# Kernel optimization log

Hardware: AMD Instinct MI355X
Metric: run time of the kernel (lower is better)

Reference implementation:

```python
import jax, jax.numpy as jnp
import numpy as np

N = 20000          # nodes
DEG = 8            # deterministic in-degree per node
E = N * DEG        # edges
IN_DIM = 16
HID = 128
EDGE_DIM = 8
OUT_DIM = 4
LN_EPS = 1e-5
# degree histogram has all mass at DEG -> avg log-degree = log(DEG + 1)
AVG_DEG_LOG = float(np.log(DEG + 1.0))


def _init(key, fan_in, fan_out):
    s = float(np.sqrt(2.0 / (fan_in + fan_out)))  # glorot-ish
    return jax.random.normal(key, (fan_in, fan_out), jnp.float32) * s


def setup_inputs() -> dict:
    key = jax.random.key(0)
    ks = jax.random.split(key, 24)
    x = jax.random.normal(ks[0], (N, IN_DIM), jnp.float32)
    src = jax.random.randint(ks[1], (E,), 0, N, jnp.int32)
    dst = (jnp.arange(E, dtype=jnp.int32) % N)  # every node has exactly DEG in-edges
    edge_index = jnp.stack([src, dst], axis=0)
    edge_attr = jax.random.normal(ks[2], (E, EDGE_DIM), jnp.float32)
    d = {"x": x, "edge_attr": edge_attr, "edge_index": edge_index}
    i = 3
    for l, fi in enumerate([IN_DIM, HID]):  # 2 PNAConv layers (num_layers=3)
        d[f"ew{l}"] = _init(ks[i], EDGE_DIM, fi); i += 1   # edge_encoder
        d[f"eb{l}"] = jnp.zeros((fi,), jnp.float32)
        d[f"pw{l}"] = _init(ks[i], 3 * fi, fi); i += 1     # pre_nn: cat(x_i,x_j,e)
        d[f"pb{l}"] = jnp.zeros((fi,), jnp.float32)
        d[f"qw{l}"] = _init(ks[i], 13 * fi, HID); i += 1   # post_nn: (4 aggr * 3 scalers + 1)*F_in
        d[f"qb{l}"] = jnp.zeros((HID,), jnp.float32)
        d[f"lw{l}"] = _init(ks[i], HID, HID); i += 1       # PNAConv.lin
        d[f"lb{l}"] = jnp.zeros((HID,), jnp.float32)
        d[f"g{l}"] = jnp.ones((HID,), jnp.float32)         # LayerNorm gamma
        d[f"b{l}"] = jnp.zeros((HID,), jnp.float32)        # LayerNorm beta
    d["hw"] = _init(ks[i], HID, OUT_DIM)
    d["hb"] = jnp.zeros((OUT_DIM,), jnp.float32)
    return d


def _pna_conv(x, src, dst, edge_attr, ew, eb, pw, pb, qw, qb, lw, lb):
    # messages: cat(x_i, x_j, edge_encoder(edge_attr)) -> pre MLP
    e = edge_attr @ ew + eb                                   # [E, F_in]
    h = jnp.concatenate([x[dst], x[src], e], axis=-1)         # [E, 3*F_in]
    h = h @ pw + pb                                           # [E, F_in]
    # multi-aggregator reduce by destination node
    deg = jax.ops.segment_sum(jnp.ones((E,), h.dtype), dst, num_segments=N)
    degc = jnp.maximum(deg, 1.0)[:, None]
    mean = jax.ops.segment_sum(h, dst, num_segments=N) / degc
    mean2 = jax.ops.segment_sum(h * h, dst, num_segments=N) / degc
    mx = jax.ops.segment_max(h, dst, num_segments=N)
    mn = jax.ops.segment_min(h, dst, num_segments=N)
    std = jnp.sqrt(jax.nn.relu(mean2 - mean * mean) + 1e-5)
    agg = jnp.concatenate([mean, mx, mn, std], axis=-1)       # [N, 4*F_in]
    # degree scalers: identity, amplification, attenuation (scaler-major layout)
    logd = jnp.log(deg + 1.0)[:, None]
    scaled = jnp.concatenate(
        [agg, agg * (logd / AVG_DEG_LOG), agg * (AVG_DEG_LOG / logd)], axis=-1
    )                                                         # [N, 12*F_in]
    out = jnp.concatenate([x, scaled], axis=-1) @ qw + qb     # post_nn, [N, F_out]
    return out @ lw + lb                                      # PNAConv.lin


def _ln(x, g, b):
    m = jnp.mean(x, axis=-1, keepdims=True)
    v = jnp.mean((x - m) ** 2, axis=-1, keepdims=True)
    return (x - m) / jnp.sqrt(v + LN_EPS) * g + b


def reference(x, edge_attr, ew0, eb0, pw0, pb0, qw0, qb0, lw0, lb0, g0, b0,
              ew1, eb1, pw1, pb1, qw1, qb1, lw1, lb1, g1, b1, hw, hb, edge_index):
    src, dst = edge_index[0], edge_index[1]
    h = _pna_conv(x, src, dst, edge_attr, ew0, eb0, pw0, pb0, qw0, qb0, lw0, lb0)
    h = jax.nn.relu(_ln(h, g0, b0))  # dropout is identity at inference
    h = _pna_conv(h, src, dst, edge_attr, ew1, eb1, pw1, pb1, qw1, qb1, lw1, lb1)
    h = jax.nn.relu(_ln(h, g1, b1))
    return h @ hw + hb               # head, [N, OUT_DIM]
```

## Files before the change

kernel.cpp:

```cpp
#include <hip/hip_runtime.h>
#include <math.h>

#define N_NODES 20000
#define N_EDGES 160000

typedef unsigned short ushort_t;
typedef __attribute__((ext_vector_type(8))) short short8v;
typedef __attribute__((ext_vector_type(4))) float f32x4;
typedef __attribute__((ext_vector_type(8))) float f32x8;

#define WS_We0  0
#define WS_b0m  128
#define WS_W0   256
#define WS_b0   10496
#define WS_We1  10624
#define WS_b1m  11648
#define WS_b1   11776
#define WS_WP1  11904
#define WS_WPTU 52864
#define WS_t0   69248
#define WS_u0   389248
#define WS_h0b  709248
#define WS_t1   1989248
#define WS_u1   4549248
#define WS_A0   7109248
#define WS_A1   7109248

__device__ inline ushort_t f2bf(float f) {
    union { float f; unsigned u; } v; v.f = f;
    unsigned r = v.u + 0x7FFFu + ((v.u >> 16) & 1u);
    return (ushort_t)(r >> 16);
}

__device__ __attribute__((noinline)) void prep_item(
    int tid, const float* __restrict__ x,
    const float* __restrict__ ew0, const float* __restrict__ eb0,
    const float* __restrict__ pw0, const float* __restrict__ pb0,
    const float* __restrict__ qw0, const float* __restrict__ qb0,
    const float* __restrict__ lw0, const float* __restrict__ lb0,
    const float* __restrict__ ew1, const float* __restrict__ eb1,
    const float* __restrict__ pw1, const float* __restrict__ pb1,
    const float* __restrict__ qw1, const float* __restrict__ qb1,
    const float* __restrict__ lw1, const float* __restrict__ lb1,
    float* __restrict__ ws)
{
    if (tid < 81920) {
        int r = tid >> 7, o = tid & 127;
        float acc = 0.f;
        for (int h = 0; h < 128; ++h) {
            float qr;
            if (r < 128) qr = qw1[r*128 + h];
            else {
                int s = r - 128;
                qr = qw1[(128+s)*128+h] + qw1[(640+s)*128+h] + qw1[(1152+s)*128+h];
            }
            acc += qr * lw1[h*128 + o];
        }
        int ct = o >> 4, ks = r >> 5;
        int l = (o & 15) | (((r >> 3) & 3) << 4);
        ((ushort_t*)(ws + WS_WP1))[(size_t)(((ct*20 + ks)*64) + l)*8 + (r & 7)] = f2bf(acc);
    } else if (tid < 82048) {
        int o = tid - 81920;
        float acc = lb1[o];
        for (int h = 0; h < 128; ++h) acc += qb1[h] * lw1[h*128 + o];
        ws[WS_b1 + o] = acc;
    } else if (tid < 92288) {
        int idx = tid - 82048; int r = idx >> 7, o = idx & 127;
        float acc = 0.f;
        for (int h = 0; h < 128; ++h) {
            float qr;
            if (r < 16) qr = qw0[r*128 + h];
            else {
                int s = r - 16;
                qr = qw0[(16+s)*128+h] + qw0[(80+s)*128+h] + qw0[(144+s)*128+h];
            }
            acc += qr * lw0[h*128 + o];
        }
        ws[WS_W0 + idx] = acc;
    } else if (tid < 92416) {
        int o = tid - 92288;
        float acc = lb0[o];
        for (int h = 0; h < 128; ++h) acc += qb0[h] * lw0[h*128 + o];
        ws[WS_b0 + o] = acc;
    } else if (tid < 93440) {
        int idx = tid - 92416; int c = idx >> 7, f = idx & 127;
        float acc = 0.f;
        for (int k = 0; k < 128; ++k) acc += ew1[c*128 + k] * pw1[(256+k)*128 + f];
        ws[WS_We1 + idx] = acc;
    } else if (tid < 93568) {
        int f = tid - 93440;
        float acc = pb1[f];
        for (int k = 0; k < 128; ++k) acc += eb1[k] * pw1[(256+k)*128 + f];
        ws[WS_b1m + f] = acc;
    } else if (tid < 93696) {
        int idx = tid - 93568; int c = idx >> 4, f = idx & 15;
        float acc = 0.f;
        for (int k = 0; k < 16; ++k) acc += ew0[c*16 + k] * pw0[(32+k)*16 + f];
        ws[WS_We0 + idx] = acc;
    } else if (tid < 93712) {
        int f = tid - 93696;
        float acc = pb0[f];
        for (int k = 0; k < 16; ++k) acc += eb0[k] * pw0[(32+k)*16 + f];
        ws[WS_b0m + f] = acc;
    } else if (tid < 126480) {
        int idx = tid - 93712;
        int r = idx >> 7, o = idx & 127;
        int part = r >> 7, rk = r & 127;
        int ct = part*8 + (o >> 4);
        int l = (o & 15) | (((rk >> 3) & 3) << 4);
        ((ushort_t*)(ws + WS_WPTU))[(size_t)(((ct*4 + (rk >> 5))*64) + l)*8 + (rk & 7)]
            = f2bf(pw1[r*128 + o]);
    } else if (tid < 446480) {
        int idx = tid - 126480; int i = idx >> 4, f = idx & 15;
        float acc = 0.f;
        for (int k = 0; k < 16; ++k) acc += x[i*16 + k] * pw0[k*16 + f];
        ws[WS_t0 + idx] = acc;
    } else if (tid < 766480) {
        int idx = tid - 446480; int i = idx >> 4, f = idx & 15;
        float acc = 0.f;
        for (int k = 0; k < 16; ++k) acc += x[i*16 + k] * pw0[(16+k)*16 + f];
        ws[WS_u0 + idx] = acc;
    }
}

__device__ __attribute__((noinline)) void agg0_tile(
    int tile, int t, const float* __restrict__ x, const float* __restrict__ ea,
    const int* __restrict__ src, float* __restrict__ ws)
{
    static __shared__ float ea_s0[16*8*8];
    static __shared__ int   src_s0[16*8];
    static __shared__ float We0_s0[128];
    static __shared__ float b0m_s0[16];
    const int i0 = tile * 16;
    __syncthreads();

    for (int idx = t; idx < 1024; idx += 256) {
        int k = idx >> 7; int rem = idx & 127; int n = rem >> 3, c = rem & 7;
        ea_s0[(n*8 + k)*8 + c] = ea[(i0 + n + k*N_NODES)*8 + c];
    }
    if (t < 128) {
        int k = t >> 4, n = t & 15;
        src_s0[n*8 + k] = src[i0 + n + k*N_NODES];
        We0_s0[t] = ws[WS_We0 + t];
    }
    if (t < 16) b0m_s0[t] = ws[WS_b0m + t];
    __syncthreads();

    const int n = t >> 4, f = t & 15;
    const int i = i0 + n;
    float base = ws[WS_t0 + i*16 + f] + b0m_s0[f];
    float s = 0.f, q = 0.f, mx = -1e30f, mn = 1e30f;
    for (int k = 0; k < 8; ++k) {
        int sj = src_s0[n*8 + k];
        float m = base + ws[WS_u0 + sj*16 + f];
        #pragma unroll
        for (int c = 0; c < 8; ++c) m += ea_s0[(n*8+k)*8 + c] * We0_s0[c*16 + f];
        s += m; q += m*m; mx = fmaxf(mx, m); mn = fminf(mn, m);
    }
    float mean = s * 0.125f, mean2 = q * 0.125f;
    float sd = sqrtf(fmaxf(mean2 - mean*mean, 0.f) + 1e-5f);
    float* A0 = ws + WS_A0 + (size_t)i * 80;
    A0[f]      = x[i*16 + f];
    A0[16 + f] = mean;
    A0[32 + f] = mx;
    A0[48 + f] = mn;
    A0[64 + f] = sd;
}

__device__ __attribute__((noinline)) void gemm0_tile(
    int tile, int t, const float* __restrict__ g0, const float* __restrict__ bln0,
    float* __restrict__ ws)
{
    static __shared__ float As[32][81];
    const int r0 = tile * 32;
    __syncthreads();
    const float* A = ws + WS_A0 + (size_t)r0 * 80;
    for (int idx = t; idx < 32*80; idx += 256) {
        int r = idx / 80, k = idx - r*80;
        As[r][k] = A[idx];
    }
    __syncthreads();
    const int tc = t & 31, tr = t >> 5;
    const int c0 = tc * 4;
    float acc[4][4] = {};
    const float* W = ws + WS_W0;
    #pragma unroll 4
    for (int k = 0; k < 80; ++k) {
        float4 b = *(const float4*)(W + k*128 + c0);
        #pragma unroll
        for (int rr = 0; rr < 4; ++rr) {
            float a = As[tr*4 + rr][k];
            acc[rr][0] += a*b.x; acc[rr][1] += a*b.y;
            acc[rr][2] += a*b.z; acc[rr][3] += a*b.w;
        }
    }
    float4 bias = *(const float4*)(ws + WS_b0 + c0);
    float4 g  = *(const float4*)(g0 + c0);
    float4 bb = *(const float4*)(bln0 + c0);
    ushort_t* h0b = (ushort_t*)(ws + WS_h0b);
    #pragma unroll
    for (int rr = 0; rr < 4; ++rr) {
        float v0 = acc[rr][0] + bias.x, v1 = acc[rr][1] + bias.y;
        float v2 = acc[rr][2] + bias.z, v3 = acc[rr][3] + bias.w;
        float sum = v0+v1+v2+v3;
        float sq  = v0*v0+v1*v1+v2*v2+v3*v3;
        #pragma unroll
        for (int off = 1; off < 32; off <<= 1) {
            sum += __shfl_xor(sum, off, 64);
            sq  += __shfl_xor(sq,  off, 64);
        }
        float mean = sum * (1.f/128.f);
        float var  = sq  * (1.f/128.f) - mean*mean;
        float rstd = rsqrtf(var + 1e-5f);
        ushort4 ob;
        ob.x = f2bf(fmaxf((v0-mean)*rstd*g.x + bb.x, 0.f));
        ob.y = f2bf(fmaxf((v1-mean)*rstd*g.y + bb.y, 0.f));
        ob.z = f2bf(fmaxf((v2-mean)*rstd*g.z + bb.z, 0.f));
        ob.w = f2bf(fmaxf((v3-mean)*rstd*g.w + bb.w, 0.f));
        *(ushort4*)(h0b + (size_t)(r0 + tr*4 + rr)*128 + c0) = ob;
    }
}

__device__ __attribute__((noinline)) void tu1_half(
    int tile, int part, int lane, float* __restrict__ ws)
{
    const int rowbase = tile * 16;
    const ushort_t* h0b = (const ushort_t*)(ws + WS_h0b);
    const ushort_t* WP  = (const ushort_t*)(ws + WS_WPTU);
    const int lr = lane & 15, lk = lane >> 4;
    const size_t arow = rowbase + lr;
    f32x4 acc[8];
    #pragma unroll
    for (int c = 0; c < 8; ++c) acc[c] = (f32x4){0.f,0.f,0.f,0.f};

    #pragma unroll
    for (int ks = 0; ks < 4; ++ks) {
        short8v a = *(const short8v*)(h0b + arow*128 + ks*32 + lk*8);
        #pragma unroll
        for (int c = 0; c < 8; ++c) {
            short8v b = *(const short8v*)(WP + ((size_t)((part*8 + c)*4 + ks)*64 + lane)*8);
            acc[c] = __builtin_amdgcn_mfma_f32_16x16x32_bf16(a, b, acc[c], 0, 0, 0);
        }
    }
    float* dst = part ? (ws + WS_u1) : (ws + WS_t1);
    #pragma unroll
    for (int c = 0; c < 8; ++c) {
        int cb = c*16 + lr;
        #pragma unroll
        for (int r = 0; r < 4; ++r) {
            int row = rowbase + lk*4 + r;
            dst[(size_t)row*128 + cb] = acc[c][r];
        }
    }
}

__device__ __attribute__((noinline)) void agg1_tile(
    int tile, int t, const float* __restrict__ ea, const int* __restrict__ src,
    float* __restrict__ ws)
{
    static __shared__ float ea_s1[16*8*8];
    static __shared__ int   src_s1[128];
    static __shared__ float We1_s1[1024];
    static __shared__ float b1m_s1[128];
    const int i0 = tile * 16;
    __syncthreads();

    for (int idx = t; idx < 1024; idx += 256) {
        int k = idx >> 7; int rem = idx & 127; int n = rem >> 3, c = rem & 7;
        ea_s1[(n*8 + k)*8 + c] = ea[(i0 + n + k*N_NODES)*8 + c];
    }
    if (t < 128) {
        int k = t >> 4, n = t & 15;
        src_s1[n*8 + k] = src[i0 + n + k*N_NODES];
    }
    for (int idx = t; idx < 1024; idx += 256) We1_s1[idx] = ws[WS_We1 + idx];
    if (t < 128) b1m_s1[t] = ws[WS_b1m + t];
    __syncthreads();

    const int n = t >> 4, f0 = (t & 15) * 8;
    const int i = i0 + n;
    float base[8], sm[8], sq[8], mx[8], mn[8];
    #pragma unroll
    for (int e = 0; e < 8; ++e) {
        base[e] = ws[WS_t1 + (size_t)i*128 + f0 + e] + b1m_s1[f0 + e];
        sm[e] = 0.f; sq[e] = 0.f; mx[e] = -1e30f; mn[e] = 1e30f;
    }
    for (int k = 0; k < 8; ++k) {
        int sj = src_s1[n*8 + k];
        const float* urow = ws + WS_u1 + (size_t)sj*128 + f0;
        float m[8];
        #pragma unroll
        for (int e = 0; e < 8; ++e) m[e] = base[e] + urow[e];
        #pragma unroll
        for (int c = 0; c < 8; ++c) {
            float a = ea_s1[(n*8 + k)*8 + c];
            #pragma unroll
            for (int e = 0; e < 8; ++e) m[e] += a * We1_s1[c*128 + f0 + e];
        }
        #pragma unroll
        for (int e = 0; e < 8; ++e) {
            sm[e] += m[e]; sq[e] += m[e]*m[e];
            mx[e] = fmaxf(mx[e], m[e]); mn[e] = fminf(mn[e], m[e]);
        }
    }
    ushort_t* A1 = (ushort_t*)(ws + WS_A1);
    short8v vm, vx, vn, vs;
    #pragma unroll
    for (int e = 0; e < 8; ++e) {
        float mean = sm[e]*0.125f, m2 = sq[e]*0.125f;
        float sd = sqrtf(fmaxf(m2 - mean*mean, 0.f) + 1e-5f);
        vm[e] = (short)f2bf(mean);
        vx[e] = (short)f2bf(mx[e]);
        vn[e] = (short)f2bf(mn[e]);
        vs[e] = (short)f2bf(sd);
    }
    size_t b = (size_t)i*512 + f0;
    *(short8v*)(A1 + b)       = vm;
    *(short8v*)(A1 + b + 128) = vx;
    *(short8v*)(A1 + b + 256) = vn;
    *(short8v*)(A1 + b + 384) = vs;
}

__device__ __attribute__((noinline)) void gemm1_tile(
    int tile, int tl, int hf,
    const float* __restrict__ g1, const float* __restrict__ bln1,
    const float* __restrict__ hw, const float* __restrict__ hb,
    float* __restrict__ ws, float* __restrict__ out)
{
    static __shared__ float redS[2][2][16], redQ[2][2][16];
    static __shared__ f32x4 redP[2][16];
    const int w = tl >> 6, lane = tl & 63;
    const int lr = lane & 15, lk = lane >> 4;
    const int rowbase = tile * 16;
    const int row = rowbase + lr;
    const ushort_t* h0b = (const ushort_t*)(ws + WS_h0b);
    const ushort_t* A1  = (const ushort_t*)(ws + WS_A1);
    const ushort_t* WP  = (const ushort_t*)(ws + WS_WP1);

    f32x4 acc[4];
    #pragma unroll
    for (int c = 0; c < 4; ++c) acc[c] = (f32x4){0.f,0.f,0.f,0.f};

    #pragma unroll
    for (int kw = 0; kw < 4; ++kw) {
        short8v a = *(const short8v*)(h0b + (size_t)row*128 + kw*32 + lk*8);
        #pragma unroll
        for (int c = 0; c < 4; ++c) {
            int ct = w*4 + c;
            short8v b = *(const short8v*)(WP + (size_t)((ct*20 + kw)*64 + lane)*8);
            acc[c] = __builtin_amdgcn_mfma_f32_16x16x32_bf16(a, b, acc[c], 0, 0, 0);
        }
    }
    #pragma unroll 4
    for (int ks = 0; ks < 16; ++ks) {
        short8v a = *(const short8v*)(A1 + (size_t)row*512 + ks*32 + lk*8);
        #pragma unroll
        for (int c = 0; c < 4; ++c) {
            int ct = w*4 + c;
            short8v b = *(const short8v*)(WP + (size_t)((ct*20 + 4 + ks)*64 + lane)*8);
            acc[c] = __builtin_amdgcn_mfma_f32_16x16x32_bf16(a, b, acc[c], 0, 0, 0);
        }
    }

    float bc[4], gc[4], bbc[4]; f32x4 hwc[4];
    #pragma unroll
    for (int c = 0; c < 4; ++c) {
        int col = (w*4 + c)*16 + lr;
        bc[c]  = ws[WS_b1 + col];
        gc[c]  = g1[col];
        bbc[c] = bln1[col];
        hwc[c] = *(const f32x4*)(hw + col*4);
    }

    #pragma unroll
    for (int r = 0; r < 4; ++r) {
        float s = 0.f, q = 0.f;
        #pragma unroll
        for (int c = 0; c < 4; ++c) {
            float v = acc[c][r] + bc[c];
            s += v; q += v*v;
        }
        #pragma unroll
        for (int off = 1; off < 16; off <<= 1) {
            s += __shfl_xor(s, off, 64);
            q += __shfl_xor(q, off, 64);
        }
        if (lr == 0) { redS[hf][w][lk*4 + r] = s; redQ[hf][w][lk*4 + r] = q; }
    }
    __syncthreads();

    f32x4 poarr[4];
    #pragma unroll
    for (int r = 0; r < 4; ++r) {
        int orow = lk*4 + r;
        float s_tot = redS[hf][0][orow] + redS[hf][1][orow];
        float q_tot = redQ[hf][0][orow] + redQ[hf][1][orow];
        float mean = s_tot * (1.f/128.f);
        float var  = q_tot * (1.f/128.f) - mean*mean;
        float rstd = rsqrtf(var + 1e-5f);
        f32x4 po = (f32x4){0.f,0.f,0.f,0.f};
        #pragma unroll
        for (int c = 0; c < 4; ++c) {
            float v = acc[c][r] + bc[c];
            float o = fmaxf((v-mean)*rstd*gc[c] + bbc[c], 0.f);
            po += o * hwc[c];
        }
        #pragma unroll
        for (int off = 1; off < 16; off <<= 1) {
            po.x += __shfl_xor(po.x, off, 64);
            po.y += __shfl_xor(po.y, off, 64);
            po.z += __shfl_xor(po.z, off, 64);
            po.w += __shfl_xor(po.w, off, 64);
        }
        poarr[r] = po;
        if (w == 1 && lr == 0) redP[hf][orow] = po;
    }
    __syncthreads();

    if (w == 0 && lr == 0) {
        f32x4 hb4 = *(const f32x4*)hb;
        #pragma unroll
        for (int r = 0; r < 4; ++r) {
            int orow = lk*4 + r;
            f32x4 res = poarr[r] + redP[hf][orow] + hb4;
            *(f32x4*)(out + (size_t)(rowbase + orow)*4) = res;
        }
    }
}

struct KArgs {
    const float *x, *ea; const int* src;
    const float *ew0,*eb0,*pw0,*pb0,*qw0,*qb0,*lw0,*lb0,*g0,*bl0;
    const float *ew1,*eb1,*pw1,*pb1,*qw1,*qb1,*lw1,*lb1,*g1,*bl1;
    const float *hw,*hb;
    float* ws; float* out;
};

__global__ __launch_bounds__(256) void k_prep(KArgs a) {
    int tid = blockIdx.x*256 + threadIdx.x;
    prep_item(tid, a.x, a.ew0, a.eb0, a.pw0, a.pb0, a.qw0, a.qb0, a.lw0, a.lb0,
              a.ew1, a.eb1, a.pw1, a.pb1, a.qw1, a.qb1, a.lw1, a.lb1, a.ws);
}

__global__ __launch_bounds__(256) void k_mid(KArgs a) {
    const int b = blockIdx.x, t = threadIdx.x;
    agg0_tile(b*2,     t, a.x, a.ea, a.src, a.ws);
    agg0_tile(b*2 + 1, t, a.x, a.ea, a.src, a.ws);
    gemm0_tile(b, t, a.g0, a.bl0, a.ws);
    __syncthreads();
    const int w = t >> 6;
    tu1_half(b*2 + (w >> 1), w & 1, t & 63, a.ws);
}

__global__ __launch_bounds__(256) void k_tail(KArgs a) {
    const int b = blockIdx.x, t = threadIdx.x;
    agg1_tile(b*2,     t, a.ea, a.src, a.ws);
    agg1_tile(b*2 + 1, t, a.ea, a.src, a.ws);
    __syncthreads();
    const int hf = t >> 7;
    gemm1_tile(b*2 + hf, t & 127, hf, a.g1, a.bl1, a.hw, a.hb, a.ws, a.out);
}

extern "C" void kernel_launch(void* const* d_in, const int* in_sizes, int n_in,
                              void* d_out, int out_size, void* d_ws, size_t ws_size,
                              hipStream_t stream)
{
    KArgs a;
    a.x    = (const float*)d_in[0];
    a.ea   = (const float*)d_in[1];
    a.src  = (const int*)d_in[2];
    a.ew0  = (const float*)d_in[3];
    a.eb0  = (const float*)d_in[4];
    a.pw0  = (const float*)d_in[5];
    a.pb0  = (const float*)d_in[6];
    a.qw0  = (const float*)d_in[7];
    a.qb0  = (const float*)d_in[8];
    a.lw0  = (const float*)d_in[9];
    a.lb0  = (const float*)d_in[10];
    a.g0   = (const float*)d_in[11];
    a.bl0  = (const float*)d_in[12];
    a.ew1  = (const float*)d_in[13];
    a.eb1  = (const float*)d_in[14];
    a.pw1  = (const float*)d_in[15];
    a.pb1  = (const float*)d_in[16];
    a.qw1  = (const float*)d_in[17];
    a.qb1  = (const float*)d_in[18];
    a.lw1  = (const float*)d_in[19];
    a.lb1  = (const float*)d_in[20];
    a.g1   = (const float*)d_in[21];
    a.bl1  = (const float*)d_in[22];
    a.hw   = (const float*)d_in[23];
    a.hb   = (const float*)d_in[24];
    a.ws   = (float*)d_ws;
    a.out  = (float*)d_out;

    k_prep<<<2995, 256, 0, stream>>>(a);
    k_mid <<< 625, 256, 0, stream>>>(a);
    k_tail<<< 625, 256, 0, stream>>>(a);
}
```

Before: 117.3 us.

## Store u1 as bf16 and split tail kernel into one tile per block

```diff
diff --git a/kernel.cpp b/kernel.cpp
--- a/kernel.cpp
+++ b/kernel.cpp
@@ -30,6 +30,9 @@
     union { float f; unsigned u; } v; v.f = f;
     unsigned r = v.u + 0x7FFFu + ((v.u >> 16) & 1u);
     return (ushort_t)(r >> 16);
+}
+__device__ inline float bf2f(short s) {
+    union { unsigned u; float f; } v; v.u = ((unsigned)(ushort_t)s) << 16; return v.f;
 }
 
 __device__ __attribute__((noinline)) void prep_item(
@@ -242,14 +245,27 @@
             acc[c] = __builtin_amdgcn_mfma_f32_16x16x32_bf16(a, b, acc[c], 0, 0, 0);
         }
     }
-    float* dst = part ? (ws + WS_u1) : (ws + WS_t1);
-    #pragma unroll
-    for (int c = 0; c < 8; ++c) {
-        int cb = c*16 + lr;
-        #pragma unroll
-        for (int r = 0; r < 4; ++r) {
-            int row = rowbase + lk*4 + r;
-            dst[(size_t)row*128 + cb] = acc[c][r];
+    if (part == 0) {
+        float* t1 = ws + WS_t1;
+        #pragma unroll
+        for (int c = 0; c < 8; ++c) {
+            int cb = c*16 + lr;
+            #pragma unroll
+            for (int r = 0; r < 4; ++r) {
+                int row = rowbase + lk*4 + r;
+                t1[(size_t)row*128 + cb] = acc[c][r];
+            }
+        }
+    } else {
+        ushort_t* u1b = (ushort_t*)(ws + WS_u1);
+        #pragma unroll
+        for (int c = 0; c < 8; ++c) {
+            int cb = c*16 + lr;
+            #pragma unroll
+            for (int r = 0; r < 4; ++r) {
+                int row = rowbase + lk*4 + r;
+                u1b[(size_t)row*128 + cb] = f2bf(acc[c][r]);
+            }
         }
     }
 }
@@ -279,6 +295,7 @@
 
     const int n = t >> 4, f0 = (t & 15) * 8;
     const int i = i0 + n;
+    const ushort_t* u1b = (const ushort_t*)(ws + WS_u1);
     float base[8], sm[8], sq[8], mx[8], mn[8];
     #pragma unroll
     for (int e = 0; e < 8; ++e) {
@@ -287,10 +304,10 @@
     }
     for (int k = 0; k < 8; ++k) {
         int sj = src_s1[n*8 + k];
-        const float* urow = ws + WS_u1 + (size_t)sj*128 + f0;
+        short8v uv = *(const short8v*)(u1b + (size_t)sj*128 + f0);
         float m[8];
         #pragma unroll
-        for (int e = 0; e < 8; ++e) m[e] = base[e] + urow[e];
+        for (int e = 0; e < 8; ++e) m[e] = base[e] + bf2f(uv[e]);
         #pragma unroll
         for (int c = 0; c < 8; ++c) {
             float a = ea_s1[(n*8 + k)*8 + c];
@@ -321,113 +338,6 @@
     *(short8v*)(A1 + b + 384) = vs;
 }
 
-__device__ __attribute__((noinline)) void gemm1_tile(
-    int tile, int tl, int hf,
-    const float* __restrict__ g1, const float* __restrict__ bln1,
-    const float* __restrict__ hw, const float* __restrict__ hb,
-    float* __restrict__ ws, float* __restrict__ out)
-{
-    static __shared__ float redS[2][2][16], redQ[2][2][16];
-    static __shared__ f32x4 redP[2][16];
-    const int w = tl >> 6, lane = tl & 63;
-    const int lr = lane & 15, lk = lane >> 4;
-    const int rowbase = tile * 16;
-    const int row = rowbase + lr;
-    const ushort_t* h0b = (const ushort_t*)(ws + WS_h0b);
-    const ushort_t* A1  = (const ushort_t*)(ws + WS_A1);
-    const ushort_t* WP  = (const ushort_t*)(ws + WS_WP1);
-
-    f32x4 acc[4];
-    #pragma unroll
-    for (int c = 0; c < 4; ++c) acc[c] = (f32x4){0.f,0.f,0.f,0.f};
-
-    #pragma unroll
-    for (int kw = 0; kw < 4; ++kw) {
-        short8v a = *(const short8v*)(h0b + (size_t)row*128 + kw*32 + lk*8);
-        #pragma unroll
-        for (int c = 0; c < 4; ++c) {
-            int ct = w*4 + c;
-            short8v b = *(const short8v*)(WP + (size_t)((ct*20 + kw)*64 + lane)*8);
-            acc[c] = __builtin_amdgcn_mfma_f32_16x16x32_bf16(a, b, acc[c], 0, 0, 0);
-        }
-    }
-    #pragma unroll 4
-    for (int ks = 0; ks < 16; ++ks) {
-        short8v a = *(const short8v*)(A1 + (size_t)row*512 + ks*32 + lk*8);
-        #pragma unroll
-        for (int c = 0; c < 4; ++c) {
-            int ct = w*4 + c;
-            short8v b = *(const short8v*)(WP + (size_t)((ct*20 + 4 + ks)*64 + lane)*8);
-            acc[c] = __builtin_amdgcn_mfma_f32_16x16x32_bf16(a, b, acc[c], 0, 0, 0);
-        }
-    }
-
-    float bc[4], gc[4], bbc[4]; f32x4 hwc[4];
-    #pragma unroll
-    for (int c = 0; c < 4; ++c) {
-        int col = (w*4 + c)*16 + lr;
-        bc[c]  = ws[WS_b1 + col];
-        gc[c]  = g1[col];
-        bbc[c] = bln1[col];
-        hwc[c] = *(const f32x4*)(hw + col*4);
-    }
-
-    #pragma unroll
-    for (int r = 0; r < 4; ++r) {
-        float s = 0.f, q = 0.f;
-        #pragma unroll
-        for (int c = 0; c < 4; ++c) {
-            float v = acc[c][r] + bc[c];
-            s += v; q += v*v;
-        }
-        #pragma unroll
-        for (int off = 1; off < 16; off <<= 1) {
-            s += __shfl_xor(s, off, 64);
-            q += __shfl_xor(q, off, 64);
-        }
-        if (lr == 0) { redS[hf][w][lk*4 + r] = s; redQ[hf][w][lk*4 + r] = q; }
-    }
-    __syncthreads();
-
-    f32x4 poarr[4];
-    #pragma unroll
-    for (int r = 0; r < 4; ++r) {
-        int orow = lk*4 + r;
-        float s_tot = redS[hf][0][orow] + redS[hf][1][orow];
-        float q_tot = redQ[hf][0][orow] + redQ[hf][1][orow];
-        float mean = s_tot * (1.f/128.f);
-        float var  = q_tot * (1.f/128.f) - mean*mean;
-        float rstd = rsqrtf(var + 1e-5f);
-        f32x4 po = (f32x4){0.f,0.f,0.f,0.f};
-        #pragma unroll
-        for (int c = 0; c < 4; ++c) {
-            float v = acc[c][r] + bc[c];
-            float o = fmaxf((v-mean)*rstd*gc[c] + bbc[c], 0.f);
-            po += o * hwc[c];
-        }
-        #pragma unroll
-        for (int off = 1; off < 16; off <<= 1) {
-            po.x += __shfl_xor(po.x, off, 64);
-            po.y += __shfl_xor(po.y, off, 64);
-            po.z += __shfl_xor(po.z, off, 64);
-            po.w += __shfl_xor(po.w, off, 64);
-        }
-        poarr[r] = po;
-        if (w == 1 && lr == 0) redP[hf][orow] = po;
-    }
-    __syncthreads();
-
-    if (w == 0 && lr == 0) {
-        f32x4 hb4 = *(const f32x4*)hb;
-        #pragma unroll
-        for (int r = 0; r < 4; ++r) {
-            int orow = lk*4 + r;
-            f32x4 res = poarr[r] + redP[hf][orow] + hb4;
-            *(f32x4*)(out + (size_t)(rowbase + orow)*4) = res;
-        }
-    }
-}
-
 struct KArgs {
     const float *x, *ea; const int* src;
     const float *ew0,*eb0,*pw0,*pb0,*qw0,*qb0,*lw0,*lb0,*g0,*bl0;
@@ -454,11 +364,108 @@
 
 __global__ __launch_bounds__(256) void k_tail(KArgs a) {
     const int b = blockIdx.x, t = threadIdx.x;
-    agg1_tile(b*2,     t, a.ea, a.src, a.ws);
-    agg1_tile(b*2 + 1, t, a.ea, a.src, a.ws);
-    __syncthreads();
-    const int hf = t >> 7;
-    gemm1_tile(b*2 + hf, t & 127, hf, a.g1, a.bl1, a.hw, a.hb, a.ws, a.out);
+    float* ws = a.ws;
+
+    agg1_tile(b, t, a.ea, a.src, ws);
+    __syncthreads();
+
+    static __shared__ float redS[4][16], redQ[4][16];
+    static __shared__ f32x4 redP[4][16];
+    const int w = t >> 6, lane = t & 63;
+    const int lr = lane & 15, lk = lane >> 4;
+    const int rowbase = b * 16;
+    const int row = rowbase + lr;
+    const ushort_t* h0b = (const ushort_t*)(ws + WS_h0b);
+    const ushort_t* A1  = (const ushort_t*)(ws + WS_A1);
+    const ushort_t* WP  = (const ushort_t*)(ws + WS_WP1);
+
+    f32x4 acc[2];
+    acc[0] = (f32x4){0.f,0.f,0.f,0.f};
+    acc[1] = (f32x4){0.f,0.f,0.f,0.f};
+
+    #pragma unroll
+    for (int kw = 0; kw < 4; ++kw) {
+        short8v av = *(const short8v*)(h0b + (size_t)row*128 + kw*32 + lk*8);
+        #pragma unroll
+        for (int c = 0; c < 2; ++c) {
+            int ct = w*2 + c;
+            short8v bv = *(const short8v*)(WP + (size_t)((ct*20 + kw)*64 + lane)*8);
+            acc[c] = __builtin_amdgcn_mfma_f32_16x16x32_bf16(av, bv, acc[c], 0, 0, 0);
+        }
+    }
+    #pragma unroll 4
+    for (int ks = 0; ks < 16; ++ks) {
+        short8v av = *(const short8v*)(A1 + (size_t)row*512 + ks*32 + lk*8);
+        #pragma unroll
+        for (int c = 0; c < 2; ++c) {
+            int ct = w*2 + c;
+            short8v bv = *(const short8v*)(WP + (size_t)((ct*20 + 4 + ks)*64 + lane)*8);
+            acc[c] = __builtin_amdgcn_mfma_f32_16x16x32_bf16(av, bv, acc[c], 0, 0, 0);
+        }
+    }
+
+    float bc[2], gc[2], bbc[2]; f32x4 hwc[2];
+    #pragma unroll
+    for (int c = 0; c < 2; ++c) {
+        int col = (w*2 + c)*16 + lr;
+        bc[c]  = ws[WS_b1 + col];
+        gc[c]  = a.g1[col];
+        bbc[c] = a.bl1[col];
+        hwc[c] = *(const f32x4*)(a.hw + col*4);
+    }
+
+    #pragma unroll
+    for (int r = 0; r < 4; ++r) {
+        float s = 0.f, q = 0.f;
+        #pragma unroll
+        for (int c = 0; c < 2; ++c) {
+            float v = acc[c][r] + bc[c];
+            s += v; q += v*v;
+        }
+        #pragma unroll
+        for (int off = 1; off < 16; off <<= 1) {
+            s += __shfl_xor(s, off, 64);
+            q += __shfl_xor(q, off, 64);
+        }
+        if (lr == 0) { redS[w][lk*4 + r] = s; redQ[w][lk*4 + r] = q; }
+    }
+    __syncthreads();
+
+    #pragma unroll
+    for (int r = 0; r < 4; ++r) {
+        int orow = lk*4 + r;
+        float s_tot = redS[0][orow] + redS[1][orow] + redS[2][orow] + redS[3][orow];
+        float q_tot = redQ[0][orow] + redQ[1][orow] + redQ[2][orow] + redQ[3][orow];
+        float mean = s_tot * (1.f/128.f);
+        float var  = q_tot * (1.f/128.f) - mean*mean;
+        float rstd = rsqrtf(var + 1e-5f);
+        f32x4 po = (f32x4){0.f,0.f,0.f,0.f};
+        #pragma unroll
+        for (int c = 0; c < 2; ++c) {
+            float v = acc[c][r] + bc[c];
+            float o = fmaxf((v-mean)*rstd*gc[c] + bbc[c], 0.f);
+            po += o * hwc[c];
+        }
+        #pragma unroll
+        for (int off = 1; off < 16; off <<= 1) {
+            po.x += __shfl_xor(po.x, off, 64);
+            po.y += __shfl_xor(po.y, off, 64);
+            po.z += __shfl_xor(po.z, off, 64);
+            po.w += __shfl_xor(po.w, off, 64);
+        }
+        if (lr == 0) redP[w][orow] = po;
+    }
+    __syncthreads();
+
+    if (w == 0 && lr == 0) {
+        f32x4 hb4 = *(const f32x4*)a.hb;
+        #pragma unroll
+        for (int r = 0; r < 4; ++r) {
+            int orow = lk*4 + r;
+            f32x4 res = redP[0][orow] + redP[1][orow] + redP[2][orow] + redP[3][orow] + hb4;
+            *(f32x4*)(a.out + (size_t)(rowbase + orow)*4) = res;
+        }
+    }
 }
 
 extern "C" void kernel_launch(void* const* d_in, const int* in_sizes, int n_in,
@@ -496,5 +503,5 @@
 
     k_prep<<<2995, 256, 0, stream>>>(a);
     k_mid <<< 625, 256, 0, stream>>>(a);
-    k_tail<<< 625, 256, 0, stream>>>(a);
-}
+    k_tail<<<1250, 256, 0, stream>>>(a);
+}
```

After: 108.5 us. 7.5% less time.
